# Kernel tuning notes

Measured on AMD Instinct MI355X. Metric: run time of the kernel, lower is better.

## Reference

```python
import jax, jax.numpy as jnp
import numpy as np

B_, S, D = 2, 2048, 2048
F_ = 8192
R = 16
H = 16
HD = D // H
MOD_SCALE = 0.1
EPS = 1e-6


def _rmsnorm(x, w):
    v = jnp.mean(x * x, axis=-1, keepdims=True)
    return x * jax.lax.rsqrt(v + EPS) * w


def setup_inputs() -> dict:
    key = jax.random.key(0)
    ks = jax.random.split(key, 12)
    sd = 0.02
    return {
        "hidden_states": jax.random.normal(ks[0], (B_, S, D), jnp.float32),
        "ln1_w": jnp.ones((D,), jnp.float32),
        "ln2_w": jnp.ones((D,), jnp.float32),
        "Wq": jax.random.normal(ks[1], (D, D), jnp.float32) * sd,
        "Wk": jax.random.normal(ks[2], (D, D), jnp.float32) * sd,
        "Wv": jax.random.normal(ks[3], (D, D), jnp.float32) * sd,
        "Wo": jax.random.normal(ks[4], (D, D), jnp.float32) * sd,
        "A": jax.random.normal(ks[5], (D, R), jnp.float32) * (0.01 / np.sqrt(D)),
        "B": jax.random.normal(ks[6], (R, F_), jnp.float32) * (0.01 / np.sqrt(R)),
        "W_in_base": jax.random.normal(ks[7], (F_, D), jnp.float32) * sd,
        "W_up_base": jax.random.normal(ks[8], (F_, D), jnp.float32) * sd,
        "W_down": jax.random.normal(ks[9], (D, F_), jnp.float32) * sd,
    }


def _attention(x, Wq, Wk, Wv, Wo):
    # x: (b, s, d). Causal multi-head self-attention, torch Linear convention (y = x @ W.T).
    b, s, d = x.shape
    q = (x @ Wq.T).reshape(b, s, H, HD)
    k = (x @ Wk.T).reshape(b, s, H, HD)
    v = (x @ Wv.T).reshape(b, s, H, HD)
    scores = jnp.einsum("bqhd,bkhd->bhqk", q, k) / np.sqrt(HD).astype(np.float32)
    causal = jnp.tril(jnp.ones((s, s), bool))
    scores = jnp.where(causal, scores, jnp.finfo(scores.dtype).min)
    probs = jax.nn.softmax(scores, axis=-1)
    out = jnp.einsum("bhqk,bkhd->bqhd", probs, v).reshape(b, s, d)
    return out @ Wo.T


def reference(hidden_states, ln1_w, ln2_w, Wq, Wk, Wv, Wo, A, B, W_in_base, W_up_base, W_down):
    residual = hidden_states
    x = _rmsnorm(hidden_states, ln1_w)
    attn = _attention(x, Wq, Wk, Wv, Wo)  # (b, s, d)

    # NeuroPlasticComponent: delta_w[b,s,d,f] = sum_r mod[b,s,r] * A[d,r] * B[r,f]
    mod = MOD_SCALE * jnp.tanh(attn @ A)  # (b, s, r)

    # NPT quirk: post_attention_layernorm is applied to the ORIGINAL residual,
    # and attention output is never added into the residual stream.
    h = _rmsnorm(residual, ln2_w)  # (b, s, d)

    # Per-token modulated gate: (W_in_base + delta_w[b,s].T) @ h
    # delta_w[b,s].T @ h = sum_d delta[d,f] h[d] = ((mod * (h @ A)) @ B)[f]
    gate_pre = h @ W_in_base.T + (mod * (h @ A)) @ B  # (b, s, f)
    gate = jax.nn.silu(gate_pre)
    up = h @ W_up_base.T
    mlp_out = (gate * up) @ W_down.T
    return residual + mlp_out
```

## Files before the change

### kernel.cpp

```cpp
#include <hip/hip_runtime.h>

#define DI __device__ __forceinline__

typedef short s16x8 __attribute__((ext_vector_type(8)));
typedef float f32x4 __attribute__((ext_vector_type(4)));

typedef __attribute__((address_space(1))) const unsigned int as1_cuint;
typedef __attribute__((address_space(3))) unsigned int as3_uint;

DI unsigned short f2bf(float f) {
  union { float f; unsigned int u; } v; v.f = f;
  unsigned int r = v.u + 0x7fffu + ((v.u >> 16) & 1u);
  return (unsigned short)(r >> 16);
}
DI float bf2f(unsigned short b) {
  union { unsigned int u; float f; } v; v.u = ((unsigned int)b) << 16;
  return v.f;
}

DI void gl_lds16(const void* g, void* l) {
  __builtin_amdgcn_global_load_lds((as1_cuint*)g, (as3_uint*)l, 16, 0, 0);
}

DI void bar() {
  __builtin_amdgcn_sched_barrier(0);
  __builtin_amdgcn_s_barrier();
  __builtin_amdgcn_sched_barrier(0);
}
DI void vm0() { asm volatile("s_waitcnt vmcnt(0)" ::: "memory"); }
DI void sfence() { __builtin_amdgcn_sched_barrier(0); }

#define MFMA __builtin_amdgcn_mfma_f32_16x16x32_bf16

__global__ __launch_bounds__(256) void cvt_f32_bf16(const float* __restrict__ src,
                                                    unsigned short* __restrict__ dst, int n4) {
  int i = blockIdx.x * blockDim.x + threadIdx.x;
  int stride = gridDim.x * blockDim.x;
  for (; i < n4; i += stride) {
    float4 v = ((const float4*)src)[i];
    ((ushort4*)dst)[i] = make_ushort4(f2bf(v.x), f2bf(v.y), f2bf(v.z), f2bf(v.w));
  }
}

__global__ __launch_bounds__(256) void rmsnorm_dual(const float* __restrict__ hs,
                                                    const float* __restrict__ w1,
                                                    const float* __restrict__ w2,
                                                    unsigned short* __restrict__ xo,
                                                    unsigned short* __restrict__ ho) {
  const int D = 2048;
  int t = blockIdx.x, tid = threadIdx.x;
  const float* row = hs + (size_t)t * D;
  float4 a = ((const float4*)row)[tid * 2];
  float4 b = ((const float4*)row)[tid * 2 + 1];
  float ss = a.x * a.x + a.y * a.y + a.z * a.z + a.w * a.w +
             b.x * b.x + b.y * b.y + b.z * b.z + b.w * b.w;
#pragma unroll
  for (int off = 32; off; off >>= 1) ss += __shfl_xor(ss, off);
  __shared__ float red[4];
  int wave = tid >> 6, lane = tid & 63;
  if (lane == 0) red[wave] = ss;
  __syncthreads();
  float tot = red[0] + red[1] + red[2] + red[3];
  float inv = rsqrtf(tot / (float)D + 1e-6f);
  int base = tid * 8;
  float vals[8] = {a.x, a.y, a.z, a.w, b.x, b.y, b.z, b.w};
  float4 w1a = ((const float4*)(w1 + base))[0];
  float4 w1b = ((const float4*)(w1 + base))[1];
  float4 w2a = ((const float4*)(w2 + base))[0];
  float4 w2b = ((const float4*)(w2 + base))[1];
  float w1v[8] = {w1a.x, w1a.y, w1a.z, w1a.w, w1b.x, w1b.y, w1b.z, w1b.w};
  float w2v[8] = {w2a.x, w2a.y, w2a.z, w2a.w, w2b.x, w2b.y, w2b.z, w2b.w};
  unsigned short ox[8], oh[8];
#pragma unroll
  for (int j = 0; j < 8; ++j) {
    float n = vals[j] * inv;
    ox[j] = f2bf(n * w1v[j]);
    oh[j] = f2bf(n * w2v[j]);
  }
  ushort4* xp = (ushort4*)(xo + (size_t)t * D + base);
  ushort4* hp = (ushort4*)(ho + (size_t)t * D + base);
  xp[0] = make_ushort4(ox[0], ox[1], ox[2], ox[3]);
  xp[1] = make_ushort4(ox[4], ox[5], ox[6], ox[7]);
  hp[0] = make_ushort4(oh[0], oh[1], oh[2], oh[3]);
  hp[1] = make_ushort4(oh[4], oh[5], oh[6], oh[7]);
}

#define E_NONE 0
#define E_RES 3

template <int EPI>
__global__ __launch_bounds__(512, 2) void gemm_n128(
    const unsigned short* __restrict__ Amat, const unsigned short* __restrict__ Bt,
    int N, int K, int NT,
    unsigned short* __restrict__ Cbf, float* __restrict__ Cf,
    const float* __restrict__ Res) {
  __shared__ __align__(16) unsigned short lds[49152];
  int tid = threadIdx.x, lane = tid & 63;
  int w = tid >> 6, wm = w >> 2, wn = w & 3;
  int lr = lane & 15, g = lane >> 4;
  int nbn = N >> 7, nwg = gridDim.x, wg = blockIdx.x;
  int cpx = nwg >> 3;
  int swz = (wg & 7) * cpx + (wg >> 3);
  int tm = swz / nbn, tn = swz - tm * nbn;
  size_t m0 = (size_t)tm * 256, n0 = (size_t)tn * 128;

  int boffA[4][2], boffB[2][2];
#pragma unroll
  for (int mi = 0; mi < 4; ++mi)
#pragma unroll
    for (int kh = 0; kh < 2; ++kh) {
      int row = mi * 32 + wm * 16 + lr;
      boffA[mi][kh] = row * 128 + ((kh * 64 + g * 16) ^ ((row & 7) << 4));
    }
#pragma unroll
  for (int ni = 0; ni < 2; ++ni)
#pragma unroll
    for (int kh = 0; kh < 2; ++kh) {
      int row = ni * 64 + wn * 16 + lr;
      boffB[ni][kh] = row * 128 + ((kh * 64 + g * 16) ^ ((row & 7) << 4));
    }
  const char* ldsb = (const char*)lds;

  int srow = tid >> 3;
  int scb = ((tid & 7) * 16) ^ ((srow & 7) << 4);
  const unsigned short* pA0 = Amat + (m0 + srow) * (size_t)K + (scb >> 1);
  const unsigned short* pA1 = pA0 + (size_t)128 * K;
  const unsigned short* pB  = Bt + (n0 + srow) * (size_t)K + (scb >> 1);
  const size_t jst = (size_t)64 * K;
  int dst = w * 512;

  f32x4 acc[8][2] = {};

  auto stg = [&](const unsigned short* p, int BUF, int SLOT) {
    gl_lds16(p, &lds[BUF * 24576 + SLOT * 8192 + dst]);
    gl_lds16(p + jst, &lds[BUF * 24576 + SLOT * 8192 + 4096 + dst]);
  };
  auto stg_all = [&](int BUF) {
    stg(pA0, BUF, 0); stg(pA1, BUF, 1); stg(pB, BUF, 2);
    pA0 += 64; pA1 += 64; pB += 64;
  };

  stg_all(0);
  vm0();
  bar();

  for (int t = 0; t < NT; ++t) {
    int BUF = t & 1;
    s16x8 afr[4][2], bfr[2][2];
#pragma unroll
    for (int mi = 0; mi < 4; ++mi)
#pragma unroll
      for (int kh = 0; kh < 2; ++kh)
        afr[mi][kh] = *(const s16x8*)(ldsb + BUF * 49152 + 0 * 16384 + boffA[mi][kh]);
#pragma unroll
    for (int ni = 0; ni < 2; ++ni)
#pragma unroll
      for (int kh = 0; kh < 2; ++kh)
        bfr[ni][kh] = *(const s16x8*)(ldsb + BUF * 49152 + 2 * 16384 + boffB[ni][kh]);
    if (t + 1 < NT) stg_all(BUF ^ 1);
    sfence();
    __builtin_amdgcn_s_setprio(1);
#pragma unroll
    for (int mi = 0; mi < 4; ++mi)
#pragma unroll
      for (int ni = 0; ni < 2; ++ni)
#pragma unroll
        for (int kh = 0; kh < 2; ++kh)
          acc[mi][ni] = MFMA(afr[mi][kh], bfr[ni][kh], acc[mi][ni], 0, 0, 0);
    __builtin_amdgcn_s_setprio(0);
    s16x8 af1[4][2];
#pragma unroll
    for (int mi = 0; mi < 4; ++mi)
#pragma unroll
      for (int kh = 0; kh < 2; ++kh)
        af1[mi][kh] = *(const s16x8*)(ldsb + BUF * 49152 + 1 * 16384 + boffA[mi][kh]);
    __builtin_amdgcn_s_setprio(1);
#pragma unroll
    for (int mi = 0; mi < 4; ++mi)
#pragma unroll
      for (int ni = 0; ni < 2; ++ni)
#pragma unroll
        for (int kh = 0; kh < 2; ++kh)
          acc[4 + mi][ni] = MFMA(af1[mi][kh], bfr[ni][kh], acc[4 + mi][ni], 0, 0, 0);
    __builtin_amdgcn_s_setprio(0);
    vm0();
    bar();
  }

#pragma unroll
  for (int mh = 0; mh < 2; ++mh)
#pragma unroll
    for (int mi = 0; mi < 4; ++mi)
#pragma unroll
      for (int r = 0; r < 4; ++r) {
        size_t row = m0 + mh * 128 + mi * 32 + wm * 16 + g * 4 + r;
#pragma unroll
        for (int ni = 0; ni < 2; ++ni) {
          size_t col = n0 + ni * 64 + wn * 16 + lr;
          float v = acc[mh * 4 + mi][ni][r];
          if constexpr (EPI == E_RES) Cf[row * N + col] = Res[row * N + col] + v;
          else Cbf[row * N + col] = f2bf(v);
        }
      }
}

__global__ __launch_bounds__(512, 2) void gemm_mlp256(
    const unsigned short* __restrict__ Hm, const unsigned short* __restrict__ Wg,
    const unsigned short* __restrict__ Wu,
    const float* __restrict__ cvec, const float* __restrict__ Bsm,
    unsigned short* __restrict__ Out) {
  const int N = 8192, K = 2048, NT = 32;
  __shared__ __align__(16) unsigned short lds[65536];
  int tid = threadIdx.x, lane = tid & 63;
  int w = tid >> 6, wm = w >> 2, wn = w & 3;
  int lr = lane & 15, g = lane >> 4;
  int nbn = N >> 7, nwg = gridDim.x, wg = blockIdx.x;
  int cpx = nwg >> 3;
  int swz = (wg & 7) * cpx + (wg >> 3);
  int tm = swz / nbn, tn = swz - tm * nbn;
  size_t m0 = (size_t)tm * 256, n0 = (size_t)tn * 128;

  int boffA[4][2], boffB[2][2];
#pragma unroll
  for (int mi = 0; mi < 4; ++mi)
#pragma unroll
    for (int kh = 0; kh < 2; ++kh) {
      int row = mi * 32 + wm * 16 + lr;
      boffA[mi][kh] = row * 128 + ((kh * 64 + g * 16) ^ ((row & 7) << 4));
    }
#pragma unroll
  for (int ni = 0; ni < 2; ++ni)
#pragma unroll
    for (int kh = 0; kh < 2; ++kh) {
      int row = ni * 64 + wn * 16 + lr;
      boffB[ni][kh] = row * 128 + ((kh * 64 + g * 16) ^ ((row & 7) << 4));
    }
  const char* ldsb = (const char*)lds;

  int srow = tid >> 3;
  int scb = ((tid & 7) * 16) ^ ((srow & 7) << 4);
  const unsigned short* pA0 = Hm + (m0 + srow) * (size_t)K + (scb >> 1);
  const unsigned short* pA1 = pA0 + (size_t)128 * K;
  const unsigned short* pBg = Wg + (n0 + srow) * (size_t)K + (scb >> 1);
  const unsigned short* pBu = Wu + (n0 + srow) * (size_t)K + (scb >> 1);
  const size_t jst = (size_t)64 * K;
  int dst = w * 512;

  f32x4 ag[8][2] = {}, au[8][2] = {};

  auto stg = [&](const unsigned short* p, int BUF, int SLOT) {
    gl_lds16(p, &lds[BUF * 32768 + SLOT * 8192 + dst]);
    gl_lds16(p + jst, &lds[BUF * 32768 + SLOT * 8192 + 4096 + dst]);
  };
  auto stg_all = [&](int BUF) {
    stg(pA0, BUF, 0); stg(pA1, BUF, 1); stg(pBg, BUF, 2); stg(pBu, BUF, 3);
    pA0 += 64; pA1 += 64; pBg += 64; pBu += 64;
  };

  stg_all(0);
  vm0();
  bar();

  for (int t = 0; t < NT; ++t) {
    int BUF = t & 1;
    s16x8 afr[4][2], bg[2][2], bu[2][2];
#pragma unroll
    for (int mi = 0; mi < 4; ++mi)
#pragma unroll
      for (int kh = 0; kh < 2; ++kh)
        afr[mi][kh] = *(const s16x8*)(ldsb + BUF * 65536 + 0 * 16384 + boffA[mi][kh]);
#pragma unroll
    for (int ni = 0; ni < 2; ++ni)
#pragma unroll
      for (int kh = 0; kh < 2; ++kh) {
        bg[ni][kh] = *(const s16x8*)(ldsb + BUF * 65536 + 2 * 16384 + boffB[ni][kh]);
        bu[ni][kh] = *(const s16x8*)(ldsb + BUF * 65536 + 3 * 16384 + boffB[ni][kh]);
      }
    if (t + 1 < NT) stg_all(BUF ^ 1);
    sfence();
    __builtin_amdgcn_s_setprio(1);
#pragma unroll
    for (int mi = 0; mi < 4; ++mi)
#pragma unroll
      for (int ni = 0; ni < 2; ++ni)
#pragma unroll
        for (int kh = 0; kh < 2; ++kh) {
          ag[mi][ni] = MFMA(afr[mi][kh], bg[ni][kh], ag[mi][ni], 0, 0, 0);
          au[mi][ni] = MFMA(afr[mi][kh], bu[ni][kh], au[mi][ni], 0, 0, 0);
        }
    __builtin_amdgcn_s_setprio(0);
    s16x8 af1[4][2];
#pragma unroll
    for (int mi = 0; mi < 4; ++mi)
#pragma unroll
      for (int kh = 0; kh < 2; ++kh)
        af1[mi][kh] = *(const s16x8*)(ldsb + BUF * 65536 + 1 * 16384 + boffA[mi][kh]);
    __builtin_amdgcn_s_setprio(1);
#pragma unroll
    for (int mi = 0; mi < 4; ++mi)
#pragma unroll
      for (int ni = 0; ni < 2; ++ni)
#pragma unroll
        for (int kh = 0; kh < 2; ++kh) {
          ag[4 + mi][ni] = MFMA(af1[mi][kh], bg[ni][kh], ag[4 + mi][ni], 0, 0, 0);
          au[4 + mi][ni] = MFMA(af1[mi][kh], bu[ni][kh], au[4 + mi][ni], 0, 0, 0);
        }
    __builtin_amdgcn_s_setprio(0);
    vm0();
    bar();
  }

  float* cl = (float*)lds;
  float* bl = (float*)&lds[32768];
#pragma unroll
  for (int j = 0; j < 2; ++j) {
    int fi = tid * 2 + j;
    ((float4*)cl)[fi] = ((const float4*)(cvec + m0 * 16))[fi];
  }
  {
    int fi = tid;
    ((float4*)bl)[fi] = *(const float4*)(Bsm + (size_t)(fi >> 5) * N + n0 + (fi & 31) * 4);
  }
  bar();

#pragma unroll
  for (int mh = 0; mh < 2; ++mh)
#pragma unroll
    for (int mi = 0; mi < 4; ++mi)
#pragma unroll
      for (int r = 0; r < 4; ++r) {
        int rr = mh * 128 + mi * 32 + wm * 16 + g * 4 + r;
        size_t row = m0 + rr;
#pragma unroll
        for (int ni = 0; ni < 2; ++ni) {
          int cc = ni * 64 + wn * 16 + lr;
          size_t col = n0 + cc;
          float s = 0.f;
#pragma unroll
          for (int jj = 0; jj < 16; ++jj) s += cl[rr * 16 + jj] * bl[jj * 128 + cc];
          float gg = ag[mh * 4 + mi][ni][r] + s;
          float sig = 1.f / (1.f + __expf(-gg));
          Out[row * N + col] = f2bf(gg * sig * au[mh * 4 + mi][ni][r]);
        }
      }
}

__global__ __launch_bounds__(256) void vtrans(const unsigned short* __restrict__ qkv,
                                              unsigned short* __restrict__ vT) {
  __shared__ unsigned short t[64][72];
  int bh = blockIdx.z, b = bh >> 4, h = bh & 15;
  int k0 = blockIdx.x * 64, d0 = blockIdx.y * 64;
  int tid = threadIdx.x;
#pragma unroll
  for (int j = 0; j < 2; ++j) {
    int idx = tid + j * 256;
    int r = idx >> 3, c8 = (idx & 7) * 8;
    s16x8 v = *(const s16x8*)(qkv + ((size_t)(b * 2048 + k0 + r)) * 6144 + 4096 + h * 128 + d0 + c8);
#pragma unroll
    for (int e = 0; e < 8; ++e) t[r][c8 + e] = (unsigned short)v[e];
  }
  __syncthreads();
#pragma unroll
  for (int j = 0; j < 2; ++j) {
    int idx = tid + j * 256;
    int dr = idx >> 3, k8 = (idx & 7) * 8;
    s16x8 o;
#pragma unroll
    for (int e = 0; e < 8; ++e) o[e] = (short)t[k8 + e][dr];
    *(s16x8*)(vT + (size_t)bh * 262144 + (size_t)(d0 + dr) * 2048 + k0 + k8) = o;
  }
}

__global__ __launch_bounds__(256, 2) void attn_fwd2(const unsigned short* __restrict__ qkv,
                                                    const unsigned short* __restrict__ vT,
                                                    unsigned short* __restrict__ attn) {
  const int LD = 6144;
  __shared__ __align__(16) unsigned short Kt[8192];
  __shared__ __align__(16) unsigned short Vt[8192];
  __shared__ __align__(16) unsigned short Pl[4096];
  int tid = threadIdx.x, w = tid >> 6, lane = tid & 63;
  int lrow = lane & 15, g = lane >> 4;
  int qp = blockIdx.x, bh = blockIdx.y, b = bh >> 4, h = bh & 15;
  const unsigned short* Qb = qkv + (size_t)b * 2048 * LD + h * 128;
  const unsigned short* Kb = Qb + 2048;
  const unsigned short* vTb = vT + (size_t)bh * 262144;
  const float scale = 0.08838834764831845f;

#pragma unroll
  for (int pass = 0; pass < 2; ++pass) {
    int qtile = pass ? (31 - qp) : qp;
    int wq0 = qtile * 64 + w * 16;
    s16x8 qf[4];
#pragma unroll
    for (int kc = 0; kc < 4; ++kc)
      qf[kc] = *(const s16x8*)(Qb + (size_t)(wq0 + lrow) * LD + kc * 32 + g * 8);
    f32x4 ao[8] = {};
    float m_r[4], l_r[4];
#pragma unroll
    for (int r = 0; r < 4; ++r) { m_r[r] = -1e30f; l_r[r] = 0.f; }
    int nkt = qtile + 1;

    for (int kt = 0; kt < nkt; ++kt) {
      int k0 = kt * 64;
      bar();
#pragma unroll
      for (int j = 0; j < 4; ++j) {
        int o = j * 4096 + tid * 16;
        int row = o >> 8, cb = o & 255;
        int scb = cb ^ ((row & 7) << 4);
        gl_lds16(Kb + (size_t)(k0 + row) * LD + (scb >> 1), &Kt[(j * 4096 + w * 1024) >> 1]);
      }
#pragma unroll
      for (int j = 0; j < 4; ++j) {
        int o = j * 4096 + tid * 16;
        int row = o >> 7, cb = o & 127;
        int scb = cb ^ ((row & 7) << 4);
        gl_lds16(vTb + (size_t)row * 2048 + k0 + (scb >> 1), &Vt[(j * 4096 + w * 1024) >> 1]);
      }
      vm0();
      bar();
      f32x4 sa[4] = {};
#pragma unroll
      for (int ni = 0; ni < 4; ++ni)
#pragma unroll
        for (int kc = 0; kc < 4; ++kc) {
          int row = ni * 16 + lrow;
          int cb = kc * 64 + g * 16;
          int scb = cb ^ ((row & 7) << 4);
          s16x8 kf = *(const s16x8*)&Kt[row * 128 + (scb >> 1)];
          sa[ni] = MFMA(qf[kc], kf, sa[ni], 0, 0, 0);
        }
      if (k0 + 63 > wq0) {
#pragma unroll
        for (int ni = 0; ni < 4; ++ni)
#pragma unroll
          for (int r = 0; r < 4; ++r) {
            int q_idx = wq0 + g * 4 + r, k_idx = k0 + ni * 16 + lrow;
            float sv = sa[ni][r] * scale;
            sa[ni][r] = (k_idx > q_idx) ? -1e30f : sv;
          }
      } else {
#pragma unroll
        for (int ni = 0; ni < 4; ++ni)
#pragma unroll
          for (int r = 0; r < 4; ++r) sa[ni][r] *= scale;
      }
      float mt[4];
#pragma unroll
      for (int r = 0; r < 4; ++r)
        mt[r] = fmaxf(fmaxf(sa[0][r], sa[1][r]), fmaxf(sa[2][r], sa[3][r]));
#pragma unroll
      for (int r = 0; r < 4; ++r)
#pragma unroll
        for (int off = 8; off; off >>= 1) mt[r] = fmaxf(mt[r], __shfl_xor(mt[r], off));
      float al[4];
#pragma unroll
      for (int r = 0; r < 4; ++r) {
        float mn = fmaxf(m_r[r], mt[r]);
        al[r] = __expf(m_r[r] - mn);
        m_r[r] = mn;
      }
      float rs[4] = {0.f, 0.f, 0.f, 0.f};
#pragma unroll
      for (int ni = 0; ni < 4; ++ni)
#pragma unroll
        for (int r = 0; r < 4; ++r) {
          float p = __expf(sa[ni][r] - m_r[r]);
          rs[r] += p;
          int q = g * 4 + r, k = ni * 16 + lrow;
          Pl[w * 1024 + q * 64 + (k ^ ((q & 7) << 3))] = f2bf(p);
        }
#pragma unroll
      for (int r = 0; r < 4; ++r) {
#pragma unroll
        for (int off = 8; off; off >>= 1) rs[r] += __shfl_xor(rs[r], off);
        l_r[r] = l_r[r] * al[r] + rs[r];
      }
#pragma unroll
      for (int df = 0; df < 8; ++df)
#pragma unroll
        for (int r = 0; r < 4; ++r) ao[df][r] *= al[r];
      asm volatile("s_waitcnt lgkmcnt(0)" ::: "memory");
      __builtin_amdgcn_sched_barrier(0);
      s16x8 pa[2];
#pragma unroll
      for (int ks = 0; ks < 2; ++ks)
        pa[ks] = *(const s16x8*)&Pl[w * 1024 + lrow * 64 + ((ks * 32 + g * 8) ^ ((lrow & 7) << 3))];
#pragma unroll
      for (int df = 0; df < 8; ++df) {
#pragma unroll
        for (int ks = 0; ks < 2; ++ks) {
          int row = df * 16 + lrow;
          int cb = ks * 64 + g * 16;
          int scb = cb ^ ((row & 7) << 4);
          s16x8 vf = *(const s16x8*)&Vt[row * 64 + (scb >> 1)];
          ao[df] = MFMA(pa[ks], vf, ao[df], 0, 0, 0);
        }
      }
    }
#pragma unroll
    for (int df = 0; df < 8; ++df)
#pragma unroll
      for (int r = 0; r < 4; ++r) {
        int q = wq0 + g * 4 + r;
        float v = ao[df][r] / l_r[r];
        attn[((size_t)b * 2048 + q) * 2048 + h * 128 + df * 16 + lrow] = f2bf(v);
      }
    bar();
  }
}

__global__ __launch_bounds__(256) void modc(const unsigned short* __restrict__ attnO,
                                            const unsigned short* __restrict__ h,
                                            const float* __restrict__ A,
                                            float* __restrict__ cvec) {
  const int D = 2048;
  int t = blockIdx.x * 4 + (threadIdx.x >> 6);
  int lane = threadIdx.x & 63;
  float aA[16] = {}, aH[16] = {};
  for (int i = 0; i < D / 64; ++i) {
    int d = i * 64 + lane;
    float av = bf2f(attnO[(size_t)t * D + d]);
    float hv = bf2f(h[(size_t)t * D + d]);
    const float* ar = A + (size_t)d * 16;
#pragma unroll
    for (int j = 0; j < 16; ++j) {
      float a = ar[j];
      aA[j] += av * a;
      aH[j] += hv * a;
    }
  }
#pragma unroll
  for (int j = 0; j < 16; ++j) {
#pragma unroll
    for (int off = 32; off; off >>= 1) {
      aA[j] += __shfl_xor(aA[j], off);
      aH[j] += __shfl_xor(aH[j], off);
    }
  }
#pragma unroll
  for (int j = 0; j < 16; ++j)
    if (lane == j) cvec[(size_t)t * 16 + j] = 0.1f * tanhf(aA[j]) * aH[j];
}

extern "C" void kernel_launch(void* const* d_in, const int* in_sizes, int n_in,
                              void* d_out, int out_size, void* d_ws, size_t ws_size,
                              hipStream_t stream) {
  const float* hs  = (const float*)d_in[0];
  const float* ln1 = (const float*)d_in[1];
  const float* ln2 = (const float*)d_in[2];
  const float* Wq  = (const float*)d_in[3];
  const float* Wk  = (const float*)d_in[4];
  const float* Wv  = (const float*)d_in[5];
  const float* Wo  = (const float*)d_in[6];
  const float* Am  = (const float*)d_in[7];
  const float* Bm  = (const float*)d_in[8];
  const float* Win = (const float*)d_in[9];
  const float* Wup = (const float*)d_in[10];
  const float* Wdn = (const float*)d_in[11];
  float* out = (float*)d_out;
  (void)in_sizes; (void)n_in;

  const int T = 4096;
  const int Dm = 2048, F = 8192;
  const size_t MB = (size_t)1 << 20;

  const size_t need = 184 * MB;
  if (ws_size < need) {
    hipMemsetAsync(d_out, 0, (size_t)out_size * 4, stream);
    return;
  }
  char* base = (char*)d_ws;
  unsigned short* tb    = (unsigned short*)(base);
  unsigned short* wqkv  = (unsigned short*)(base);
  unsigned short* vT    = (unsigned short*)(base);
  unsigned short* xb    = (unsigned short*)(base + 24 * MB);
  unsigned short* attnO = (unsigned short*)(base + 40 * MB);
  unsigned short* qkv   = (unsigned short*)(base + 64 * MB);
  unsigned short* win   = (unsigned short*)(base + 64 * MB);
  unsigned short* wo    = (unsigned short*)(base + 112 * MB);
  unsigned short* hb    = (unsigned short*)(base + 120 * MB);
  unsigned short* attn  = (unsigned short*)(base + 136 * MB);
  float*          cv    = (float*)(base + 136 * MB);
  unsigned short* wup   = (unsigned short*)(base + 152 * MB);
  unsigned short* wdn   = (unsigned short*)(base + 152 * MB);

  cvt_f32_bf16<<<2048, 256, 0, stream>>>(Wq, wqkv, Dm * Dm / 4);
  cvt_f32_bf16<<<2048, 256, 0, stream>>>(Wk, wqkv + (size_t)Dm * Dm, Dm * Dm / 4);
  cvt_f32_bf16<<<2048, 256, 0, stream>>>(Wv, wqkv + (size_t)2 * Dm * Dm, Dm * Dm / 4);
  cvt_f32_bf16<<<2048, 256, 0, stream>>>(Wo, wo, Dm * Dm / 4);
  rmsnorm_dual<<<T, 256, 0, stream>>>(hs, ln1, ln2, xb, hb);

  gemm_n128<E_NONE><<<(T / 256) * (3 * Dm / 128), 512, 0, stream>>>(
      xb, wqkv, 3 * Dm, Dm, Dm / 64, qkv, nullptr, nullptr);

  vtrans<<<dim3(32, 2, 32), 256, 0, stream>>>(qkv, vT);
  attn_fwd2<<<dim3(16, 32), 256, 0, stream>>>(qkv, vT, attn);

  gemm_n128<E_NONE><<<(T / 256) * (Dm / 128), 512, 0, stream>>>(
      attn, wo, Dm, Dm, Dm / 64, attnO, nullptr, nullptr);

  modc<<<T / 4, 256, 0, stream>>>(attnO, hb, Am, cv);

  cvt_f32_bf16<<<2048, 256, 0, stream>>>(Win, win, F * Dm / 4);
  cvt_f32_bf16<<<2048, 256, 0, stream>>>(Wup, wup, F * Dm / 4);

  gemm_mlp256<<<(T / 256) * (F / 128), 512, 0, stream>>>(hb, win, wup, cv, Bm, tb);

  cvt_f32_bf16<<<2048, 256, 0, stream>>>(Wdn, wdn, Dm * F / 4);
  gemm_n128<E_RES><<<(T / 256) * (Dm / 128), 512, 0, stream>>>(
      tb, wdn, Dm, F, F / 64, nullptr, out, hs);
}
```

Before: 773.8 us.

## Drop LDS double buffering in GEMMs and shrink MLP tile to 128x128

The gemm_n128 kernel and the fused gate/up MLP GEMM both switch from double-buffered LDS prefetch to a single buffer that is loaded, waited on and then consumed each K step. The MLP kernel also changes from 512-thread 256x128 tiles to 256-thread 128x128 tiles with a new warp layout, so it uses far less LDS and launches twice as many blocks. The aim is higher occupancy and more resident blocks per CU. The cost is that global-to-LDS loads no longer overlap with MFMA work inside a block, so stalls per K step go up.

Result: slower. 965.7 us (+24.8%).

```diff
diff --git a/kernel.cpp b/kernel.cpp
--- a/kernel.cpp
+++ b/kernel.cpp
@@ -131,34 +131,31 @@
 
   f32x4 acc[8][2] = {};
 
-  auto stg = [&](const unsigned short* p, int BUF, int SLOT) {
-    gl_lds16(p, &lds[BUF * 24576 + SLOT * 8192 + dst]);
-    gl_lds16(p + jst, &lds[BUF * 24576 + SLOT * 8192 + 4096 + dst]);
+  auto stg = [&](const unsigned short* p, int SLOT) {
+    gl_lds16(p, &lds[SLOT * 8192 + dst]);
+    gl_lds16(p + jst, &lds[SLOT * 8192 + 4096 + dst]);
   };
-  auto stg_all = [&](int BUF) {
-    stg(pA0, BUF, 0); stg(pA1, BUF, 1); stg(pB, BUF, 2);
+  auto stg_all = [&]() {
+    stg(pA0, 0); stg(pA1, 1); stg(pB, 2);
     pA0 += 64; pA1 += 64; pB += 64;
   };
 
-  stg_all(0);
-  vm0();
-  bar();
-
   for (int t = 0; t < NT; ++t) {
-    int BUF = t & 1;
+    bar();
+    stg_all();
+    vm0();
+    bar();
     s16x8 afr[4][2], bfr[2][2];
 #pragma unroll
     for (int mi = 0; mi < 4; ++mi)
 #pragma unroll
       for (int kh = 0; kh < 2; ++kh)
-        afr[mi][kh] = *(const s16x8*)(ldsb + BUF * 49152 + 0 * 16384 + boffA[mi][kh]);
+        afr[mi][kh] = *(const s16x8*)(ldsb + 0 * 16384 + boffA[mi][kh]);
 #pragma unroll
     for (int ni = 0; ni < 2; ++ni)
 #pragma unroll
       for (int kh = 0; kh < 2; ++kh)
-        bfr[ni][kh] = *(const s16x8*)(ldsb + BUF * 49152 + 2 * 16384 + boffB[ni][kh]);
-    if (t + 1 < NT) stg_all(BUF ^ 1);
-    sfence();
+        bfr[ni][kh] = *(const s16x8*)(ldsb + 2 * 16384 + boffB[ni][kh]);
     __builtin_amdgcn_s_setprio(1);
 #pragma unroll
     for (int mi = 0; mi < 4; ++mi)
@@ -173,7 +170,7 @@
     for (int mi = 0; mi < 4; ++mi)
 #pragma unroll
       for (int kh = 0; kh < 2; ++kh)
-        af1[mi][kh] = *(const s16x8*)(ldsb + BUF * 49152 + 1 * 16384 + boffA[mi][kh]);
+        af1[mi][kh] = *(const s16x8*)(ldsb + 1 * 16384 + boffA[mi][kh]);
     __builtin_amdgcn_s_setprio(1);
 #pragma unroll
     for (int mi = 0; mi < 4; ++mi)
@@ -183,8 +180,6 @@
         for (int kh = 0; kh < 2; ++kh)
           acc[4 + mi][ni] = MFMA(af1[mi][kh], bfr[ni][kh], acc[4 + mi][ni], 0, 0, 0);
     __builtin_amdgcn_s_setprio(0);
-    vm0();
-    bar();
   }
 
 #pragma unroll
@@ -204,145 +199,120 @@
       }
 }
 
-__global__ __launch_bounds__(512, 2) void gemm_mlp256(
+__global__ __launch_bounds__(256, 2) void gemm_mlp_db(
     const unsigned short* __restrict__ Hm, const unsigned short* __restrict__ Wg,
     const unsigned short* __restrict__ Wu,
     const float* __restrict__ cvec, const float* __restrict__ Bsm,
     unsigned short* __restrict__ Out) {
   const int N = 8192, K = 2048, NT = 32;
-  __shared__ __align__(16) unsigned short lds[65536];
+  __shared__ __align__(16) unsigned short lds[24576];
   int tid = threadIdx.x, lane = tid & 63;
-  int w = tid >> 6, wm = w >> 2, wn = w & 3;
+  int w = tid >> 6;
   int lr = lane & 15, g = lane >> 4;
   int nbn = N >> 7, nwg = gridDim.x, wg = blockIdx.x;
   int cpx = nwg >> 3;
   int swz = (wg & 7) * cpx + (wg >> 3);
   int tm = swz / nbn, tn = swz - tm * nbn;
-  size_t m0 = (size_t)tm * 256, n0 = (size_t)tn * 128;
-
-  int boffA[4][2], boffB[2][2];
-#pragma unroll
-  for (int mi = 0; mi < 4; ++mi)
+  size_t m0 = (size_t)tm * 128, n0 = (size_t)tn * 128;
+
+  int boffA[8][2], boffBg[2][2], boffBu[2][2];
+#pragma unroll
+  for (int mi = 0; mi < 8; ++mi)
 #pragma unroll
     for (int kh = 0; kh < 2; ++kh) {
-      int row = mi * 32 + wm * 16 + lr;
+      int row = mi * 16 + lr;
       boffA[mi][kh] = row * 128 + ((kh * 64 + g * 16) ^ ((row & 7) << 4));
     }
 #pragma unroll
   for (int ni = 0; ni < 2; ++ni)
 #pragma unroll
     for (int kh = 0; kh < 2; ++kh) {
-      int row = ni * 64 + wn * 16 + lr;
-      boffB[ni][kh] = row * 128 + ((kh * 64 + g * 16) ^ ((row & 7) << 4));
+      int row = w * 32 + ni * 16 + lr;
+      int sz = row * 128 + ((kh * 64 + g * 16) ^ ((row & 7) << 4));
+      boffBg[ni][kh] = 16384 + sz;
+      boffBu[ni][kh] = 32768 + sz;
     }
   const char* ldsb = (const char*)lds;
 
-  int srow = tid >> 3;
-  int scb = ((tid & 7) * 16) ^ ((srow & 7) << 4);
-  const unsigned short* pA0 = Hm + (m0 + srow) * (size_t)K + (scb >> 1);
-  const unsigned short* pA1 = pA0 + (size_t)128 * K;
-  const unsigned short* pBg = Wg + (n0 + srow) * (size_t)K + (scb >> 1);
-  const unsigned short* pBu = Wu + (n0 + srow) * (size_t)K + (scb >> 1);
-  const size_t jst = (size_t)64 * K;
-  int dst = w * 512;
+  const unsigned short* sp[12];
+#pragma unroll
+  for (int i = 0; i < 12; ++i) {
+    int c = i * 256 + tid;
+    const unsigned short* gb;
+    size_t r0;
+    int lrow;
+    if (i < 4)      { gb = Hm; r0 = m0; lrow = c >> 3; }
+    else if (i < 8) { gb = Wg; r0 = n0; lrow = (c - 1024) >> 3; }
+    else            { gb = Wu; r0 = n0; lrow = (c - 2048) >> 3; }
+    int cb = (c & 7) * 16;
+    int scb = cb ^ ((lrow & 7) << 4);
+    sp[i] = gb + (r0 + lrow) * (size_t)K + (scb >> 1);
+  }
 
   f32x4 ag[8][2] = {}, au[8][2] = {};
 
-  auto stg = [&](const unsigned short* p, int BUF, int SLOT) {
-    gl_lds16(p, &lds[BUF * 32768 + SLOT * 8192 + dst]);
-    gl_lds16(p + jst, &lds[BUF * 32768 + SLOT * 8192 + 4096 + dst]);
-  };
-  auto stg_all = [&](int BUF) {
-    stg(pA0, BUF, 0); stg(pA1, BUF, 1); stg(pBg, BUF, 2); stg(pBu, BUF, 3);
-    pA0 += 64; pA1 += 64; pBg += 64; pBu += 64;
-  };
-
-  stg_all(0);
-  vm0();
-  bar();
-
   for (int t = 0; t < NT; ++t) {
-    int BUF = t & 1;
-    s16x8 afr[4][2], bg[2][2], bu[2][2];
-#pragma unroll
-    for (int mi = 0; mi < 4; ++mi)
-#pragma unroll
-      for (int kh = 0; kh < 2; ++kh)
-        afr[mi][kh] = *(const s16x8*)(ldsb + BUF * 65536 + 0 * 16384 + boffA[mi][kh]);
-#pragma unroll
-    for (int ni = 0; ni < 2; ++ni)
-#pragma unroll
-      for (int kh = 0; kh < 2; ++kh) {
-        bg[ni][kh] = *(const s16x8*)(ldsb + BUF * 65536 + 2 * 16384 + boffB[ni][kh]);
-        bu[ni][kh] = *(const s16x8*)(ldsb + BUF * 65536 + 3 * 16384 + boffB[ni][kh]);
-      }
-    if (t + 1 < NT) stg_all(BUF ^ 1);
-    sfence();
-    __builtin_amdgcn_s_setprio(1);
-#pragma unroll
-    for (int mi = 0; mi < 4; ++mi)
-#pragma unroll
-      for (int ni = 0; ni < 2; ++ni)
-#pragma unroll
-        for (int kh = 0; kh < 2; ++kh) {
-          ag[mi][ni] = MFMA(afr[mi][kh], bg[ni][kh], ag[mi][ni], 0, 0, 0);
-          au[mi][ni] = MFMA(afr[mi][kh], bu[ni][kh], au[mi][ni], 0, 0, 0);
-        }
-    __builtin_amdgcn_s_setprio(0);
-    s16x8 af1[4][2];
-#pragma unroll
-    for (int mi = 0; mi < 4; ++mi)
-#pragma unroll
-      for (int kh = 0; kh < 2; ++kh)
-        af1[mi][kh] = *(const s16x8*)(ldsb + BUF * 65536 + 1 * 16384 + boffA[mi][kh]);
-    __builtin_amdgcn_s_setprio(1);
-#pragma unroll
-    for (int mi = 0; mi < 4; ++mi)
-#pragma unroll
-      for (int ni = 0; ni < 2; ++ni)
-#pragma unroll
-        for (int kh = 0; kh < 2; ++kh) {
-          ag[4 + mi][ni] = MFMA(af1[mi][kh], bg[ni][kh], ag[4 + mi][ni], 0, 0, 0);
-          au[4 + mi][ni] = MFMA(af1[mi][kh], bu[ni][kh], au[4 + mi][ni], 0, 0, 0);
-        }
-    __builtin_amdgcn_s_setprio(0);
+    bar();
+#pragma unroll
+    for (int i = 0; i < 12; ++i) {
+      gl_lds16(sp[i], &lds[i * 2048 + w * 512]);
+      sp[i] += 64;
+    }
     vm0();
     bar();
-  }
-
+    s16x8 bg[2][2], bu[2][2];
+#pragma unroll
+    for (int ni = 0; ni < 2; ++ni)
+#pragma unroll
+      for (int kh = 0; kh < 2; ++kh) {
+        bg[ni][kh] = *(const s16x8*)(ldsb + boffBg[ni][kh]);
+        bu[ni][kh] = *(const s16x8*)(ldsb + boffBu[ni][kh]);
+      }
+    __builtin_amdgcn_s_setprio(1);
+#pragma unroll
+    for (int mi = 0; mi < 8; ++mi) {
+      s16x8 a0 = *(const s16x8*)(ldsb + boffA[mi][0]);
+      s16x8 a1 = *(const s16x8*)(ldsb + boffA[mi][1]);
+#pragma unroll
+      for (int ni = 0; ni < 2; ++ni) {
+        ag[mi][ni] = MFMA(a0, bg[ni][0], ag[mi][ni], 0, 0, 0);
+        ag[mi][ni] = MFMA(a1, bg[ni][1], ag[mi][ni], 0, 0, 0);
+        au[mi][ni] = MFMA(a0, bu[ni][0], au[mi][ni], 0, 0, 0);
+        au[mi][ni] = MFMA(a1, bu[ni][1], au[mi][ni], 0, 0, 0);
+      }
+    }
+    __builtin_amdgcn_s_setprio(0);
+  }
+
+  bar();
   float* cl = (float*)lds;
-  float* bl = (float*)&lds[32768];
+  float* bl = (float*)&lds[4096];
 #pragma unroll
   for (int j = 0; j < 2; ++j) {
     int fi = tid * 2 + j;
     ((float4*)cl)[fi] = ((const float4*)(cvec + m0 * 16))[fi];
-  }
-  {
-    int fi = tid;
     ((float4*)bl)[fi] = *(const float4*)(Bsm + (size_t)(fi >> 5) * N + n0 + (fi & 31) * 4);
   }
-  bar();
-
-#pragma unroll
-  for (int mh = 0; mh < 2; ++mh)
-#pragma unroll
-    for (int mi = 0; mi < 4; ++mi)
-#pragma unroll
-      for (int r = 0; r < 4; ++r) {
-        int rr = mh * 128 + mi * 32 + wm * 16 + g * 4 + r;
-        size_t row = m0 + rr;
-#pragma unroll
-        for (int ni = 0; ni < 2; ++ni) {
-          int cc = ni * 64 + wn * 16 + lr;
-          size_t col = n0 + cc;
-          float s = 0.f;
-#pragma unroll
-          for (int jj = 0; jj < 16; ++jj) s += cl[rr * 16 + jj] * bl[jj * 128 + cc];
-          float gg = ag[mh * 4 + mi][ni][r] + s;
-          float sig = 1.f / (1.f + __expf(-gg));
-          Out[row * N + col] = f2bf(gg * sig * au[mh * 4 + mi][ni][r]);
-        }
-      }
+  __syncthreads();
+
+#pragma unroll
+  for (int mi = 0; mi < 8; ++mi)
+#pragma unroll
+    for (int r = 0; r < 4; ++r) {
+      int rr = mi * 16 + g * 4 + r;
+      size_t row = m0 + rr;
+#pragma unroll
+      for (int ni = 0; ni < 2; ++ni) {
+        int cc = w * 32 + ni * 16 + lr;
+        size_t col = n0 + cc;
+        float s = 0.f;
+#pragma unroll
+        for (int jj = 0; jj < 16; ++jj) s += cl[rr * 16 + jj] * bl[jj * 128 + cc];
+        float gg = ag[mi][ni][r] + s;
+        float sig = 1.f / (1.f + __expf(-gg));
+        Out[row * N + col] = f2bf(gg * sig * au[mi][ni][r]);
+      }
+    }
 }
 
 __global__ __launch_bounds__(256) void vtrans(const unsigned short* __restrict__ qkv,
@@ -605,7 +575,7 @@
   cvt_f32_bf16<<<2048, 256, 0, stream>>>(Win, win, F * Dm / 4);
   cvt_f32_bf16<<<2048, 256, 0, stream>>>(Wup, wup, F * Dm / 4);
 
-  gemm_mlp256<<<(T / 256) * (F / 128), 512, 0, stream>>>(hb, win, wup, cv, Bm, tb);
+  gemm_mlp_db<<<(T / 128) * (F / 128), 256, 0, stream>>>(hb, win, wup, cv, Bm, tb);
 
   cvt_f32_bf16<<<2048, 256, 0, stream>>>(Wdn, wdn, Dm * F / 4);
   gemm_n128<E_RES><<<(T / 256) * (Dm / 128), 512, 0, stream>>>(
```
